# Kernel optimization log

Measured on AMD Instinct MI355X. Metric: run time of the kernel, lower is better.

The kernel has to match this reference:

```python
import jax, jax.numpy as jnp
import numpy as np

B, T, D = 64, 8192, 16   # batch, time, state dim
H = 128                  # recurr_size
HID = (256, 256)         # MLP hidden sizes
OUT = 1                  # output_dim
F = D + 1                # features + weight channel


def setup_inputs() -> dict:
    key = jax.random.key(0)
    ks = jax.random.split(key, 12)
    s = lambda k, shp: jax.random.normal(k, shp, jnp.float32) * 0.05
    return {
        "particles": jax.random.normal(ks[0], (B, T, D), jnp.float32),
        "weights": jax.random.uniform(ks[1], (B, T), jnp.float32),
        # GRU params: packed [r|z|n] gates; input dense has no bias (flax GRUCell),
        # hidden dense has bias.
        "Wi": s(ks[2], (F, 3 * H)),
        "Wh": s(ks[3], (H, 3 * H)),
        "bh": jnp.zeros((3 * H,), jnp.float32),
        # MLP decoder params
        "W1": s(ks[4], (H, HID[0])), "b1": jnp.zeros((HID[0],), jnp.float32),
        "W2": s(ks[5], (HID[0], HID[1])), "b2": jnp.zeros((HID[1],), jnp.float32),
        "W3": s(ks[6], (HID[1], OUT)), "b3": jnp.zeros((OUT,), jnp.float32),
        # log_std param, initialized with ones (init_log_std default)
        "log_std": jnp.ones((OUT,), jnp.float32),
    }


def _gru_last(inputs, Wi, Wh, bh):
    """Run GRU over time (axis 1 of [B,T,F]); return final hidden state [B,H].
    Equivalent to taking encoding at the last timestep."""
    h0 = jnp.zeros((inputs.shape[0], H), inputs.dtype)

    def step(h, x_t):  # x_t: [B,F]
        gi = x_t @ Wi              # [B,3H], no input bias (flax GRUCell)
        gh = h @ Wh + bh           # [B,3H]
        ir, iz, inn = jnp.split(gi, 3, axis=-1)
        hr, hz, hn = jnp.split(gh, 3, axis=-1)
        r = jax.nn.sigmoid(ir + hr)
        z = jax.nn.sigmoid(iz + hz)
        n = jnp.tanh(inn + r * hn)
        h_new = (1.0 - z) * n + z * h
        return h_new, None

    xs = jnp.swapaxes(inputs, 0, 1)  # [T,B,F]
    h_last, _ = jax.lax.scan(step, h0, xs)
    return h_last


def reference(particles, weights, Wi, Wh, bh, W1, b1, W2, b2, W3, b3, log_std):
    features = particles  # feature_fn = identity
    inputs = jnp.concatenate([features, weights[..., None]], axis=-1)  # [B,T,F]
    enc = _gru_last(inputs, Wi, Wh, bh)  # [B,H] == encoding at last timestep
    x = jax.nn.relu(enc @ W1 + b1)
    x = jax.nn.relu(x @ W2 + b2)
    mean = x @ W3 + b3  # [B,OUT]
    return mean, log_std
```

## Files before the change

kernel.cpp:

```cpp
#include <hip/hip_runtime.h>
#include <hip/hip_bf16.h>

#define B 64
#define T 8192
#define D 16
#define H 128
#define F 17
#define NTHREADS 512
#define CHUNK 32
#define XSTR 40

typedef _Float16 half_t;
typedef _Float16 f16x8 __attribute__((ext_vector_type(8)));
typedef _Float16 f16x4 __attribute__((ext_vector_type(4)));
typedef float f32x4 __attribute__((ext_vector_type(4)));

#define MFMA(a, b, c) __builtin_amdgcn_mfma_f32_16x16x32_f16((a), (b), (c), 0, 0, 0)

__device__ __forceinline__ float fast_rcp(float x) {
#if __has_builtin(__builtin_amdgcn_rcpf)
  return __builtin_amdgcn_rcpf(x);
#else
  return 1.0f / x;
#endif
}
__device__ __forceinline__ float fast_exp2(float x) {
#if __has_builtin(__builtin_amdgcn_exp2f)
  return __builtin_amdgcn_exp2f(x);
#else
  return exp2f(x);
#endif
}

#define GSTEP(RB, WB, TT)                                                    \
  do {                                                                       \
    const f16x8* hv = (const f16x8*)(RB);                                    \
    f16x8 a0 = hv[mg], a1 = hv[4 + mg], a2 = hv[8 + mg], a3 = hv[12 + mg];   \
    f16x4 gv = *(const f16x4*)(gi_lds + (((TT) & 31) * H + jj) * 4);         \
    const float gr = (float)gv[0], gz = (float)gv[1], gin = (float)gv[2];    \
    f32x4 ar = {gr, gr, gr, gr};                                             \
    f32x4 az = {gz, gz, gz, gz};                                             \
    f32x4 an = {bn, bn, bn, bn};                                             \
    ar = MFMA(a0, wr0, ar); az = MFMA(a0, wz0, az); an = MFMA(a0, wn0, an);  \
    ar = MFMA(a1, wr1, ar); az = MFMA(a1, wz1, az); an = MFMA(a1, wn1, an);  \
    ar = MFMA(a2, wr2, ar); az = MFMA(a2, wz2, az); an = MFMA(a2, wn2, an);  \
    ar = MFMA(a3, wr3, ar); az = MFMA(a3, wz3, az); an = MFMA(a3, wn3, an);  \
    float rr = fast_rcp(1.0f + fast_exp2(-ar[0]));                           \
    float zz = fast_rcp(1.0f + fast_exp2(-az[0]));                           \
    float pre = fmaf(rr, an[0], gin);                                        \
    pre = fminf(fmaxf(pre, -40.0f), 40.0f);                                  \
    float e = fast_exp2(-pre);                                               \
    float nn = (1.0f - e) * fast_rcp(1.0f + e);                              \
    hreg = fmaf(zz, hreg - nn, nn);                       \
    if (mg == 0) (WB)[jj] = (half_t)hreg;                                    \
    __syncthreads();                                                         \
  } while (0)

__global__ __launch_bounds__(NTHREADS, 1)
void policy_gru_kernel(const float* __restrict__ particles,
                       const float* __restrict__ weights,
                       const float* __restrict__ Wi, const float* __restrict__ Wh,
                       const float* __restrict__ bh,
                       const float* __restrict__ W1, const float* __restrict__ b1,
                       const float* __restrict__ W2, const float* __restrict__ b2,
                       const float* __restrict__ W3, const float* __restrict__ b3,
                       const float* __restrict__ log_std,
                       float* __restrict__ out)
{
  __shared__ __align__(16) half_t hb[2][H];
  __shared__ __align__(16) half_t xs[CHUNK * XSTR];
  __shared__ __align__(16) half_t gi_lds[CHUNK * H * 4];
  __shared__ float sg[NTHREADS];
  __shared__ float red[8];

  const int tid = threadIdx.x;
  const int b   = blockIdx.x;
  const int l   = tid & 63;
  const int w   = tid >> 6;
  const int mg  = l >> 4;
  const int jn  = l & 15;
  const int jj  = w * 16 + jn;

  const float L1 = 1.4426950408889634f;
  const float L2 = 2.0f * L1;

  auto wload = [&](int gate, int s) -> f16x8 {
    f16x8 v;
    const float sc  = (gate == 2) ? L2 : L1;
    const int   col = gate * H + jj;
    #pragma unroll
    for (int r = 0; r < 8; ++r) {
      const int k = s * 32 + mg * 8 + r;
      v[r] = (half_t)(Wh[k * 384 + col] * sc);
    }
    return v;
  };
  const f16x8 wr0 = wload(0,0), wr1 = wload(0,1), wr2 = wload(0,2), wr3 = wload(0,3);
  const f16x8 wz0 = wload(1,0), wz1 = wload(1,1), wz2 = wload(1,2), wz3 = wload(1,3);
  const f16x8 wn0 = wload(2,0), wn1 = wload(2,1), wn2 = wload(2,2), wn3 = wload(2,3);

  auto wiload = [&](int gate) -> f16x8 {
    f16x8 v;
    const float sc  = (gate == 2) ? L2 : L1;
    const int   col = gate * H + jj;
    #pragma unroll
    for (int i = 0; i < 8; ++i) {
      const int k = mg * 8 + i;
      v[i] = (half_t)(k < F ? Wi[k * 384 + col] * sc : 0.0f);
    }
    return v;
  };
  const f16x8 wiR = wiload(0), wiZ = wiload(1), wiN = wiload(2);
  const float br = bh[jj] * L1, bz = bh[128 + jj] * L1, bn = bh[256 + jj] * L2;

  const int e0 = tid, e1 = tid + NTHREADS;
  float xr0 = 0.f, xr1 = 0.f;
  auto xfetch = [&](int t0) {
    auto ld = [&](int e) -> float {
      const int tau = e / F, f = e % F;
      int t = t0 + tau; if (t > T - 1) t = T - 1;
      return (f < D) ? particles[((size_t)b * T + t) * D + f]
                     : weights[(size_t)b * T + t];
    };
    xr0 = ld(e0);
    if (e1 < CHUNK * F) xr1 = ld(e1);
  };
  auto xstage = [&]() {
    xs[(e0 / F) * XSTR + (e0 % F)] = (half_t)xr0;
    if (e1 < CHUNK * F) xs[(e1 / F) * XSTR + (e1 % F)] = (half_t)xr1;
  };

  auto gi_compute = [&]() {
    f16x8 aX0 = *(const f16x8*)(xs + (jn     ) * XSTR + mg * 8);
    f16x8 aX1 = *(const f16x8*)(xs + (jn + 16) * XSTR + mg * 8);
    f32x4 cr0 = {br, br, br, br}, cz0 = {bz, bz, bz, bz}, cn0 = {0.f,0.f,0.f,0.f};
    f32x4 cr1 = cr0, cz1 = cz0, cn1 = cn0;
    cr0 = MFMA(aX0, wiR, cr0); cz0 = MFMA(aX0, wiZ, cz0); cn0 = MFMA(aX0, wiN, cn0);
    cr1 = MFMA(aX1, wiR, cr1); cz1 = MFMA(aX1, wiZ, cz1); cn1 = MFMA(aX1, wiN, cn1);
    #pragma unroll
    for (int r = 0; r < 4; ++r) {
      const int t0r = (l >> 4) * 4 + r;
      gi_lds[(t0r * H + jj) * 4 + 0] = (half_t)cr0[r];
      gi_lds[(t0r * H + jj) * 4 + 1] = (half_t)cz0[r];
      gi_lds[(t0r * H + jj) * 4 + 2] = (half_t)cn0[r];
      const int t1r = t0r + 16;
      gi_lds[(t1r * H + jj) * 4 + 0] = (half_t)cr1[r];
      gi_lds[(t1r * H + jj) * 4 + 1] = (half_t)cz1[r];
      gi_lds[(t1r * H + jj) * 4 + 2] = (half_t)cn1[r];
    }
  };

  float hreg = 0.0f;
  if (tid < H) { hb[0][tid] = (half_t)0.f; hb[1][tid] = (half_t)0.f; }
  for (int i = tid; i < CHUNK * XSTR; i += NTHREADS) xs[i] = (half_t)0.f;
  xfetch(0);
  __syncthreads();
  xstage();
  xfetch(CHUNK);
  __syncthreads();
  gi_compute();
  __syncthreads();

  for (int t0 = 0; t0 < T; t0 += CHUNK) {
    #pragma unroll 4
    for (int tt = 0; tt < CHUNK; tt += 2) {
      GSTEP(hb[0], hb[1], tt);
      GSTEP(hb[1], hb[0], tt + 1);
    }
    if (t0 + CHUNK < T) {
      xstage();
      xfetch(t0 + 2 * CHUNK);
      __syncthreads();
      gi_compute();
      __syncthreads();
    }
  }

  if (mg == 0) sg[jj] = hreg;
  __syncthreads();

  float a1 = 0.0f;
  if (tid < 256) {
    a1 = b1[tid];
    #pragma unroll 4
    for (int k = 0; k < H; ++k) a1 = fmaf(sg[k], W1[k * 256 + tid], a1);
    a1 = fmaxf(a1, 0.0f);
    sg[256 + tid] = a1;
  }
  __syncthreads();

  float a2 = 0.0f;
  if (tid < 256) {
    a2 = b2[tid];
    #pragma unroll 4
    for (int k = 0; k < 256; ++k) a2 = fmaf(sg[256 + k], W2[k * 256 + tid], a2);
    a2 = fmaxf(a2, 0.0f);
    a2 *= W3[tid];
  }
  #pragma unroll
  for (int off = 32; off > 0; off >>= 1) a2 += __shfl_down(a2, off, 64);
  if (tid < 256 && (tid & 63) == 0) red[tid >> 6] = a2;
  __syncthreads();
  if (tid == 0) {
    out[b] = red[0] + red[1] + red[2] + red[3] + b3[0];
    if (b == 0) out[B] = log_std[0];
  }
}

extern "C" void kernel_launch(void* const* d_in, const int* in_sizes, int n_in,
                              void* d_out, int out_size, void* d_ws, size_t ws_size,
                              hipStream_t stream) {
  const float* particles = (const float*)d_in[0];
  const float* weights   = (const float*)d_in[1];
  const float* Wi      = (const float*)d_in[2];
  const float* Wh      = (const float*)d_in[3];
  const float* bh      = (const float*)d_in[4];
  const float* W1      = (const float*)d_in[5];
  const float* b1      = (const float*)d_in[6];
  const float* W2      = (const float*)d_in[7];
  const float* b2      = (const float*)d_in[8];
  const float* W3      = (const float*)d_in[9];
  const float* b3      = (const float*)d_in[10];
  const float* log_std = (const float*)d_in[11];

  policy_gru_kernel<<<dim3(B), dim3(NTHREADS), 0, stream>>>(
      particles, weights, Wi, Wh, bh, W1, b1, W2, b2, W3, b3, log_std,
      (float*)d_out);
}
```

Before: 3.040 ms.

## Replace per-step MFMA recurrent matvec with packed fp16 dot2 plus cross-lane reduction

```diff
diff --git a/kernel.cpp b/kernel.cpp
--- a/kernel.cpp
+++ b/kernel.cpp
@@ -9,10 +9,11 @@
 #define NTHREADS 512
 #define CHUNK 32
 #define XSTR 40
+#define GSTR 516
 
 typedef _Float16 half_t;
 typedef _Float16 f16x8 __attribute__((ext_vector_type(8)));
-typedef _Float16 f16x4 __attribute__((ext_vector_type(4)));
+typedef _Float16 f16x2 __attribute__((ext_vector_type(2)));
 typedef float f32x4 __attribute__((ext_vector_type(4)));
 
 #define MFMA(a, b, c) __builtin_amdgcn_mfma_f32_16x16x32_f16((a), (b), (c), 0, 0, 0)
@@ -31,23 +32,45 @@
   return exp2f(x);
 #endif
 }
+__device__ __forceinline__ float fdot2(f16x2 a, f16x2 b, float c) {
+#if __has_builtin(__builtin_amdgcn_fdot2)
+  return __builtin_amdgcn_fdot2(a, b, c, false);
+#else
+  return c + (float)a.x * (float)b.x + (float)a.y * (float)b.y;
+#endif
+}
+__device__ __forceinline__ f16x2 pick2(f16x8 v, int i) {
+  return f16x2{v[2 * i], v[2 * i + 1]};
+}
 
 #define GSTEP(RB, WB, TT)                                                    \
   do {                                                                       \
-    const f16x8* hv = (const f16x8*)(RB);                                    \
-    f16x8 a0 = hv[mg], a1 = hv[4 + mg], a2 = hv[8 + mg], a3 = hv[12 + mg];   \
-    f16x4 gv = *(const f16x4*)(gi_lds + (((TT) & 31) * H + jj) * 4);         \
-    const float gr = (float)gv[0], gz = (float)gv[1], gin = (float)gv[2];    \
-    f32x4 ar = {gr, gr, gr, gr};                                             \
-    f32x4 az = {gz, gz, gz, gz};                                             \
-    f32x4 an = {bn, bn, bn, bn};                                             \
-    ar = MFMA(a0, wr0, ar); az = MFMA(a0, wz0, az); an = MFMA(a0, wn0, an);  \
-    ar = MFMA(a1, wr1, ar); az = MFMA(a1, wz1, az); an = MFMA(a1, wn1, an);  \
-    ar = MFMA(a2, wr2, ar); az = MFMA(a2, wz2, az); an = MFMA(a2, wn2, an);  \
-    ar = MFMA(a3, wr3, ar); az = MFMA(a3, wz3, az); an = MFMA(a3, wn3, an);  \
-    float rr = fast_rcp(1.0f + fast_exp2(-ar[0]));                           \
-    float zz = fast_rcp(1.0f + fast_exp2(-az[0]));                           \
-    float pre = fmaf(rr, an[0], gin);                                        \
+    const f32x4 gv = *(const f32x4*)(gi_lds + ((TT) & 31) * GSTR + jj * 4);  \
+    const f16x8* hp = (const f16x8*)((RB) + mg * 32);                        \
+    const f16x8 hA = hp[0], hB = hp[1], hC = hp[2], hD = hp[3];              \
+    float r0=0,r1=0,r2=0,r3=0, z0=0,z1=0,z2=0,z3=0, n0=0,n1=0,n2=0,n3=0;     \
+    _Pragma("unroll")                                                        \
+    for (int i = 0; i < 4; ++i) {                                            \
+      f16x2 pA = pick2(hA, i), pB = pick2(hB, i),                            \
+            pC = pick2(hC, i), pD = pick2(hD, i);                            \
+      r0 = fdot2(pA, whr[i     ], r0); z0 = fdot2(pA, whz[i     ], z0);      \
+      n0 = fdot2(pA, whn[i     ], n0);                                       \
+      r1 = fdot2(pB, whr[i +  4], r1); z1 = fdot2(pB, whz[i +  4], z1);      \
+      n1 = fdot2(pB, whn[i +  4], n1);                                       \
+      r2 = fdot2(pC, whr[i +  8], r2); z2 = fdot2(pC, whz[i +  8], z2);      \
+      n2 = fdot2(pC, whn[i +  8], n2);                                       \
+      r3 = fdot2(pD, whr[i + 12], r3); z3 = fdot2(pD, whz[i + 12], z3);      \
+      n3 = fdot2(pD, whn[i + 12], n3);                                       \
+    }                                                                        \
+    float sr = (r0 + r1) + (r2 + r3);                                        \
+    float sz = (z0 + z1) + (z2 + z3);                                        \
+    float sn = (n0 + n1) + (n2 + n3);                                        \
+    sr += __shfl_xor(sr, 16, 64); sr += __shfl_xor(sr, 32, 64);              \
+    sz += __shfl_xor(sz, 16, 64); sz += __shfl_xor(sz, 32, 64);              \
+    sn += __shfl_xor(sn, 16, 64); sn += __shfl_xor(sn, 32, 64);              \
+    float rr = fast_rcp(1.0f + fast_exp2(-(sr + gv[0])));                    \
+    float zz = fast_rcp(1.0f + fast_exp2(-(sz + gv[1])));                    \
+    float pre = fmaf(rr, sn + bn2, gv[2]);                                   \
     pre = fminf(fmaxf(pre, -40.0f), 40.0f);                                  \
     float e = fast_exp2(-pre);                                               \
     float nn = (1.0f - e) * fast_rcp(1.0f + e);                              \
@@ -69,7 +92,7 @@
 {
   __shared__ __align__(16) half_t hb[2][H];
   __shared__ __align__(16) half_t xs[CHUNK * XSTR];
-  __shared__ __align__(16) half_t gi_lds[CHUNK * H * 4];
+  __shared__ __align__(16) float gi_lds[CHUNK * GSTR];
   __shared__ float sg[NTHREADS];
   __shared__ float red[8];
 
@@ -84,20 +107,18 @@
   const float L1 = 1.4426950408889634f;
   const float L2 = 2.0f * L1;
 
-  auto wload = [&](int gate, int s) -> f16x8 {
-    f16x8 v;
-    const float sc  = (gate == 2) ? L2 : L1;
-    const int   col = gate * H + jj;
-    #pragma unroll
-    for (int r = 0; r < 8; ++r) {
-      const int k = s * 32 + mg * 8 + r;
-      v[r] = (half_t)(Wh[k * 384 + col] * sc);
-    }
-    return v;
-  };
-  const f16x8 wr0 = wload(0,0), wr1 = wload(0,1), wr2 = wload(0,2), wr3 = wload(0,3);
-  const f16x8 wz0 = wload(1,0), wz1 = wload(1,1), wz2 = wload(1,2), wz3 = wload(1,3);
-  const f16x8 wn0 = wload(2,0), wn1 = wload(2,1), wn2 = wload(2,2), wn3 = wload(2,3);
+  f16x2 whr[16], whz[16], whn[16];
+  #pragma unroll
+  for (int i = 0; i < 16; ++i) {
+    const int k = mg * 32 + 2 * i;
+    whr[i] = f16x2{(half_t)(Wh[k * 384 + jj] * L1),
+                   (half_t)(Wh[(k + 1) * 384 + jj] * L1)};
+    whz[i] = f16x2{(half_t)(Wh[k * 384 + 128 + jj] * L1),
+                   (half_t)(Wh[(k + 1) * 384 + 128 + jj] * L1)};
+    whn[i] = f16x2{(half_t)(Wh[k * 384 + 256 + jj] * L2),
+                   (half_t)(Wh[(k + 1) * 384 + 256 + jj] * L2)};
+  }
+  const float bn2 = bh[256 + jj] * L2;
 
   auto wiload = [&](int gate) -> f16x8 {
     f16x8 v;
@@ -111,7 +132,7 @@
     return v;
   };
   const f16x8 wiR = wiload(0), wiZ = wiload(1), wiN = wiload(2);
-  const float br = bh[jj] * L1, bz = bh[128 + jj] * L1, bn = bh[256 + jj] * L2;
+  const float br = bh[jj] * L1, bz = bh[128 + jj] * L1;
 
   const int e0 = tid, e1 = tid + NTHREADS;
   float xr0 = 0.f, xr1 = 0.f;
@@ -139,14 +160,12 @@
     cr1 = MFMA(aX1, wiR, cr1); cz1 = MFMA(aX1, wiZ, cz1); cn1 = MFMA(aX1, wiN, cn1);
     #pragma unroll
     for (int r = 0; r < 4; ++r) {
-      const int t0r = (l >> 4) * 4 + r;
-      gi_lds[(t0r * H + jj) * 4 + 0] = (half_t)cr0[r];
-      gi_lds[(t0r * H + jj) * 4 + 1] = (half_t)cz0[r];
-      gi_lds[(t0r * H + jj) * 4 + 2] = (half_t)cn0[r];
+      const int t0r = mg * 4 + r;
+      f32x4 v0 = {cr0[r], cz0[r], cn0[r], 0.f};
+      *(f32x4*)(gi_lds + t0r * GSTR + jj * 4) = v0;
       const int t1r = t0r + 16;
-      gi_lds[(t1r * H + jj) * 4 + 0] = (half_t)cr1[r];
-      gi_lds[(t1r * H + jj) * 4 + 1] = (half_t)cz1[r];
-      gi_lds[(t1r * H + jj) * 4 + 2] = (half_t)cn1[r];
+      f32x4 v1 = {cr1[r], cz1[r], cn1[r], 0.f};
+      *(f32x4*)(gi_lds + t1r * GSTR + jj * 4) = v1;
     }
   };
 
@@ -162,7 +181,6 @@
   __syncthreads();
 
   for (int t0 = 0; t0 < T; t0 += CHUNK) {
-    #pragma unroll 4
     for (int tt = 0; tt < CHUNK; tt += 2) {
       GSTEP(hb[0], hb[1], tt);
       GSTEP(hb[1], hb[0], tt + 1);
@@ -176,7 +194,7 @@
     }
   }
 
-  if (mg == 0) sg[jj] = hreg;
+  if (mg == 0 && w < 8) sg[jj] = hreg;
   __syncthreads();
 
   float a1 = 0.0f;
```

Result: slower. 4.482 ms (+47.5%).

## Quantize recurrent GRU matmul to FP8 with scaled 16x16x128 MFMA

Applied to the files above, without the earlier changes.

```diff
diff --git a/kernel.cpp b/kernel.cpp
--- a/kernel.cpp
+++ b/kernel.cpp
@@ -1,5 +1,6 @@
 #include <hip/hip_runtime.h>
 #include <hip/hip_bf16.h>
+#include <hip/hip_fp8.h>
 
 #define B 64
 #define T 8192
@@ -9,13 +10,16 @@
 #define NTHREADS 512
 #define CHUNK 32
 #define XSTR 40
+#define GSTR 516
 
 typedef _Float16 half_t;
 typedef _Float16 f16x8 __attribute__((ext_vector_type(8)));
-typedef _Float16 f16x4 __attribute__((ext_vector_type(4)));
 typedef float f32x4 __attribute__((ext_vector_type(4)));
+typedef int i32x8 __attribute__((ext_vector_type(8)));
 
 #define MFMA(a, b, c) __builtin_amdgcn_mfma_f32_16x16x32_f16((a), (b), (c), 0, 0, 0)
+#define MFMAS(a, b, c) \
+  __builtin_amdgcn_mfma_scale_f32_16x16x128_f8f6f4((a), (b), (c), 0, 0, 0, 0x7F7F7F7F, 0, 0x7F7F7F7F)
 
 __device__ __forceinline__ float fast_rcp(float x) {
 #if __has_builtin(__builtin_amdgcn_rcpf)
@@ -31,28 +35,29 @@
   return exp2f(x);
 #endif
 }
+__device__ __forceinline__ unsigned char f32_to_e4m3(float f) {
+  __hip_fp8_e4m3 q(f);
+  return __builtin_bit_cast(unsigned char, q);
+}
 
 #define GSTEP(RB, WB, TT)                                                    \
   do {                                                                       \
-    const f16x8* hv = (const f16x8*)(RB);                                    \
-    f16x8 a0 = hv[mg], a1 = hv[4 + mg], a2 = hv[8 + mg], a3 = hv[12 + mg];   \
-    f16x4 gv = *(const f16x4*)(gi_lds + (((TT) & 31) * H + jj) * 4);         \
-    const float gr = (float)gv[0], gz = (float)gv[1], gin = (float)gv[2];    \
-    f32x4 ar = {gr, gr, gr, gr};                                             \
-    f32x4 az = {gz, gz, gz, gz};                                             \
-    f32x4 an = {bn, bn, bn, bn};                                             \
-    ar = MFMA(a0, wr0, ar); az = MFMA(a0, wz0, az); an = MFMA(a0, wn0, an);  \
-    ar = MFMA(a1, wr1, ar); az = MFMA(a1, wz1, az); an = MFMA(a1, wn1, an);  \
-    ar = MFMA(a2, wr2, ar); az = MFMA(a2, wz2, az); an = MFMA(a2, wn2, an);  \
-    ar = MFMA(a3, wr3, ar); az = MFMA(a3, wz3, az); an = MFMA(a3, wn3, an);  \
+    const f32x4 gv = *(const f32x4*)(gi_lds + ((TT) & 31) * GSTR + jj * 4);  \
+    const i32x8 a8 = *(const i32x8*)((RB) + mg * 32);                        \
+    f32x4 ar = {gv[0], gv[0], gv[0], gv[0]};                                 \
+    f32x4 az = {gv[1], gv[1], gv[1], gv[1]};                                 \
+    f32x4 an = {bn2, bn2, bn2, bn2};                                         \
+    ar = MFMAS(a8, wb_r, ar);                                                \
+    az = MFMAS(a8, wb_z, az);                                                \
+    an = MFMAS(a8, wb_n, an);                                                \
     float rr = fast_rcp(1.0f + fast_exp2(-ar[0]));                           \
     float zz = fast_rcp(1.0f + fast_exp2(-az[0]));                           \
-    float pre = fmaf(rr, an[0], gin);                                        \
+    float pre = fmaf(rr, an[0], gv[2]);                                      \
     pre = fminf(fmaxf(pre, -40.0f), 40.0f);                                  \
     float e = fast_exp2(-pre);                                               \
     float nn = (1.0f - e) * fast_rcp(1.0f + e);                              \
     hreg = fmaf(zz, hreg - nn, nn);                       \
-    if (mg == 0) (WB)[jj] = (half_t)hreg;                                    \
+    if (mg == 0) (WB)[jj] = f32_to_e4m3(hreg);                               \
     __syncthreads();                                                         \
   } while (0)
 
@@ -67,9 +72,9 @@
                        const float* __restrict__ log_std,
                        float* __restrict__ out)
 {
-  __shared__ __align__(16) half_t hb[2][H];
+  __shared__ __align__(32) unsigned char hb8[2][H];
   __shared__ __align__(16) half_t xs[CHUNK * XSTR];
-  __shared__ __align__(16) half_t gi_lds[CHUNK * H * 4];
+  __shared__ __align__(16) float gi_lds[CHUNK * GSTR];
   __shared__ float sg[NTHREADS];
   __shared__ float red[8];
 
@@ -84,20 +89,24 @@
   const float L1 = 1.4426950408889634f;
   const float L2 = 2.0f * L1;
 
-  auto wload = [&](int gate, int s) -> f16x8 {
-    f16x8 v;
+  auto wload8 = [&](int gate) -> i32x8 {
     const float sc  = (gate == 2) ? L2 : L1;
     const int   col = gate * H + jj;
+    i32x8 v;
     #pragma unroll
     for (int r = 0; r < 8; ++r) {
-      const int k = s * 32 + mg * 8 + r;
-      v[r] = (half_t)(Wh[k * 384 + col] * sc);
+      unsigned int word = 0;
+      #pragma unroll
+      for (int byt = 0; byt < 4; ++byt) {
+        const int k = mg * 32 + r * 4 + byt;
+        word |= ((unsigned int)f32_to_e4m3(Wh[k * 384 + col] * sc)) << (8 * byt);
+      }
+      v[r] = (int)word;
     }
     return v;
   };
-  const f16x8 wr0 = wload(0,0), wr1 = wload(0,1), wr2 = wload(0,2), wr3 = wload(0,3);
-  const f16x8 wz0 = wload(1,0), wz1 = wload(1,1), wz2 = wload(1,2), wz3 = wload(1,3);
-  const f16x8 wn0 = wload(2,0), wn1 = wload(2,1), wn2 = wload(2,2), wn3 = wload(2,3);
+  const i32x8 wb_r = wload8(0), wb_z = wload8(1), wb_n = wload8(2);
+  const float bn2 = bh[256 + jj] * L2;
 
   auto wiload = [&](int gate) -> f16x8 {
     f16x8 v;
@@ -111,7 +120,7 @@
     return v;
   };
   const f16x8 wiR = wiload(0), wiZ = wiload(1), wiN = wiload(2);
-  const float br = bh[jj] * L1, bz = bh[128 + jj] * L1, bn = bh[256 + jj] * L2;
+  const float br = bh[jj] * L1, bz = bh[128 + jj] * L1;
 
   const int e0 = tid, e1 = tid + NTHREADS;
   float xr0 = 0.f, xr1 = 0.f;
@@ -139,19 +148,17 @@
     cr1 = MFMA(aX1, wiR, cr1); cz1 = MFMA(aX1, wiZ, cz1); cn1 = MFMA(aX1, wiN, cn1);
     #pragma unroll
     for (int r = 0; r < 4; ++r) {
-      const int t0r = (l >> 4) * 4 + r;
-      gi_lds[(t0r * H + jj) * 4 + 0] = (half_t)cr0[r];
-      gi_lds[(t0r * H + jj) * 4 + 1] = (half_t)cz0[r];
-      gi_lds[(t0r * H + jj) * 4 + 2] = (half_t)cn0[r];
+      const int t0r = mg * 4 + r;
+      f32x4 v0 = {cr0[r], cz0[r], cn0[r], 0.f};
+      *(f32x4*)(gi_lds + t0r * GSTR + jj * 4) = v0;
       const int t1r = t0r + 16;
-      gi_lds[(t1r * H + jj) * 4 + 0] = (half_t)cr1[r];
-      gi_lds[(t1r * H + jj) * 4 + 1] = (half_t)cz1[r];
-      gi_lds[(t1r * H + jj) * 4 + 2] = (half_t)cn1[r];
+      f32x4 v1 = {cr1[r], cz1[r], cn1[r], 0.f};
+      *(f32x4*)(gi_lds + t1r * GSTR + jj * 4) = v1;
     }
   };
 
   float hreg = 0.0f;
-  if (tid < H) { hb[0][tid] = (half_t)0.f; hb[1][tid] = (half_t)0.f; }
+  if (tid < H) { hb8[0][tid] = 0; hb8[1][tid] = 0; }
   for (int i = tid; i < CHUNK * XSTR; i += NTHREADS) xs[i] = (half_t)0.f;
   xfetch(0);
   __syncthreads();
@@ -162,10 +169,9 @@
   __syncthreads();
 
   for (int t0 = 0; t0 < T; t0 += CHUNK) {
-    #pragma unroll 4
     for (int tt = 0; tt < CHUNK; tt += 2) {
-      GSTEP(hb[0], hb[1], tt);
-      GSTEP(hb[1], hb[0], tt + 1);
+      GSTEP(hb8[0], hb8[1], tt);
+      GSTEP(hb8[1], hb8[0], tt + 1);
     }
     if (t0 + CHUNK < T) {
       xstage();
```

Result: faster. 2.584 ms (-15.0%).
